# Performance work log

Measured on AMD Instinct MI355X. Metric: run time of the kernel, lower is better.

## Reference

```python
import jax, jax.numpy as jnp
import numpy as np

D_MODEL = 1024
N_HEADS = 16
D_HEAD = D_MODEL // N_HEADS
D_FF = 4096
BATCH = 2
SEQ = 2048
LN_EPS = 1e-5


def setup_inputs() -> dict:
    key = jax.random.key(0)
    ks = jax.random.split(key, 12)
    s = 1.0 / np.sqrt(D_MODEL)
    x = jax.random.normal(ks[0], (BATCH, SEQ, D_MODEL), dtype=jnp.float32)
    mask = jnp.broadcast_to(jnp.tril(jnp.ones((SEQ, SEQ), jnp.int32)), (BATCH, SEQ, SEQ))
    return {
        "x": x,
        "mask": mask,
        # per-head projections stacked: [H, D, Dh] (bias=False in source)
        "Wq": jax.random.normal(ks[1], (N_HEADS, D_MODEL, D_HEAD), jnp.float32) * s,
        "Wk": jax.random.normal(ks[2], (N_HEADS, D_MODEL, D_HEAD), jnp.float32) * s,
        "Wv": jax.random.normal(ks[3], (N_HEADS, D_MODEL, D_HEAD), jnp.float32) * s,
        "Wo": jax.random.normal(ks[4], (D_MODEL, D_MODEL), jnp.float32) * s,
        "ln1_w": jnp.ones((D_MODEL,), jnp.float32),
        "ln1_b": jnp.zeros((D_MODEL,), jnp.float32),
        "ln2_w": jnp.ones((D_MODEL,), jnp.float32),
        "ln2_b": jnp.zeros((D_MODEL,), jnp.float32),
        "W1": jax.random.normal(ks[5], (D_MODEL, D_FF), jnp.float32) * s,
        "b1": jnp.zeros((D_FF,), jnp.float32),
        "W2": jax.random.normal(ks[6], (D_FF, D_MODEL), jnp.float32) * (1.0 / np.sqrt(D_FF)),
        "b2": jnp.zeros((D_MODEL,), jnp.float32),
    }


def layer_norm(x, w, b):
    mu = jnp.mean(x, axis=-1, keepdims=True)
    var = jnp.var(x, axis=-1, keepdims=True)
    return (x - mu) * jax.lax.rsqrt(var + LN_EPS) * w + b


def reference(x, mask, Wq, Wk, Wv, Wo, ln1_w, ln1_b, ln2_w, ln2_b, W1, b1, W2, b2):
    # pre-LN masked self-attention
    h = layer_norm(x, ln1_w, ln1_b)
    q = jnp.einsum("bsd,hde->bhse", h, Wq)  # [B,H,S,Dh]
    k = jnp.einsum("bsd,hde->bhse", h, Wk)
    v = jnp.einsum("bsd,hde->bhse", h, Wv)
    scores = jnp.einsum("bhse,bhte->bhst", q, k) / np.sqrt(D_HEAD)
    scores = jnp.where(mask[:, None, :, :].astype(bool), scores, -jnp.inf)
    weights = jax.nn.softmax(scores, axis=-1)
    attn = jnp.einsum("bhst,bhte->bhse", weights, v)  # [B,H,S,Dh]
    # concat heads (head order = last-dim order in torch.cat)
    concat = attn.transpose(0, 2, 1, 3).reshape(x.shape[0], x.shape[1], D_MODEL)
    att_out = concat @ Wo
    att_x = x + att_out
    # FFN with exact (erf) GELU, matching nn.GELU default
    h2 = layer_norm(att_x, ln2_w, ln2_b)
    ff = jax.nn.gelu(h2 @ W1 + b1, approximate=False) @ W2 + b2
    return att_x + ff
```

## Files before the change

### kernel.cpp

```cpp
#include <hip/hip_runtime.h>
#include <hip/hip_bf16.h>
#include <math.h>

#define D_MODEL 1024
#define N_HEADS 16
#define D_HEAD  64
#define D_FF    4096
#define BATCH   2
#define SEQ     2048
#define NTOK    (BATCH*SEQ)

typedef __hip_bfloat16 bf16;
typedef __attribute__((ext_vector_type(8))) short short8;
typedef __attribute__((ext_vector_type(4))) float floatx4;

template<typename TIN>
__global__ void ln_kernel(const TIN* __restrict__ x,
                          const float* __restrict__ w,
                          const float* __restrict__ b,
                          bf16* __restrict__ out) {
    int row = blockIdx.x;
    int tid = threadIdx.x;
    const long base = (long)row * D_MODEL;
    float v[4];
    float s = 0.f, sq = 0.f;
#pragma unroll
    for (int i = 0; i < 4; ++i) {
        float xv = (float)x[base + tid + i*256];
        v[i] = xv; s += xv; sq += xv*xv;
    }
    __shared__ float r1[256], r2[256];
    r1[tid] = s; r2[tid] = sq; __syncthreads();
    for (int off = 128; off > 0; off >>= 1) {
        if (tid < off) { r1[tid] += r1[tid+off]; r2[tid] += r2[tid+off]; }
        __syncthreads();
    }
    float mean = r1[0] * (1.f/D_MODEL);
    float var  = r2[0] * (1.f/D_MODEL) - mean*mean;
    float rstd = rsqrtf(var + 1e-5f);
#pragma unroll
    for (int i = 0; i < 4; ++i) {
        int c = tid + i*256;
        out[base + c] = __float2bfloat16((v[i] - mean) * rstd * w[c] + b[c]);
    }
}

__global__ __launch_bounds__(256) void wcvt_kernel(const float* __restrict__ W,
                                                   bf16* __restrict__ Wt,
                                                   int K, int N) {
    __shared__ float t[32][33];
    int n0 = blockIdx.x * 32, k0 = blockIdx.y * 32;
    int lx = threadIdx.x & 31, ly = threadIdx.x >> 5;
#pragma unroll
    for (int i = 0; i < 4; ++i) {
        int k = ly + i * 8;
        t[k][lx] = W[(long)(k0 + k) * N + n0 + lx];
    }
    __syncthreads();
#pragma unroll
    for (int i = 0; i < 4; ++i) {
        int n = ly + i * 8;
        Wt[(long)(n0 + n) * K + k0 + lx] = __float2bfloat16(t[lx][n]);
    }
}

__global__ __launch_bounds__(256) void wcvt_wo_w1(const float* __restrict__ Wo,
                                                  const float* __restrict__ W1,
                                                  bf16* __restrict__ wo_bf,
                                                  bf16* __restrict__ w1_bf) {
    __shared__ float t[32][33];
    int gx = blockIdx.x;
    const float* W; bf16* Wt; int N, n0;
    if (gx < 32) { W = Wo; Wt = wo_bf; N = D_MODEL; n0 = gx * 32; }
    else         { W = W1; Wt = w1_bf; N = D_FF;    n0 = (gx - 32) * 32; }
    int k0 = blockIdx.y * 32;
    int lx = threadIdx.x & 31, ly = threadIdx.x >> 5;
#pragma unroll
    for (int i = 0; i < 4; ++i) {
        int k = ly + i * 8;
        t[k][lx] = W[(long)(k0 + k) * N + n0 + lx];
    }
    __syncthreads();
#pragma unroll
    for (int i = 0; i < 4; ++i) {
        int n = ly + i * 8;
        Wt[(long)(n0 + n) * D_MODEL + k0 + lx] = __float2bfloat16(t[lx][n]);
    }
}

__global__ __launch_bounds__(256) void wcvt_qkv(const float* __restrict__ Wq,
                                                const float* __restrict__ Wk,
                                                const float* __restrict__ Wv,
                                                bf16* __restrict__ outp) {
    __shared__ float t[32][33];
    int z = blockIdx.z, mat = z >> 4, head = z & 15;
    const float* W = (mat == 0 ? Wq : mat == 1 ? Wk : Wv) + (long)head * D_MODEL * D_HEAD;
    bf16* Wt = outp + (long)z * D_HEAD * D_MODEL;
    int n0 = blockIdx.x * 32, k0 = blockIdx.y * 32;
    int lx = threadIdx.x & 31, ly = threadIdx.x >> 5;
#pragma unroll
    for (int i = 0; i < 4; ++i) {
        int k = ly + i * 8;
        t[k][lx] = W[(long)(k0 + k) * D_HEAD + n0 + lx];
    }
    __syncthreads();
#pragma unroll
    for (int i = 0; i < 4; ++i) {
        int n = ly + i * 8;
        Wt[(long)(n0 + n) * D_MODEL + k0 + lx] = __float2bfloat16(t[lx][n]);
    }
}

__device__ inline void swz2d(int& bx, int& by) {
    int gx = gridDim.x;
    int nwg = gx * gridDim.y;
    int bid = blockIdx.y * gx + blockIdx.x;
    int swz = (bid & 7) * (nwg >> 3) + (bid >> 3);
    bx = swz % gx;
    by = swz / gx;
}

template<int ROWS>
__device__ inline void stage_tile(const bf16* g, int gstride, short* lds) {
    int lane = threadIdx.x & 63, wave = threadIdx.x >> 6;
#pragma unroll
    for (int it = 0; it < ROWS / 64; ++it) {
        int c = wave + it * 4;
        const bf16* gp = g + (long)(c * 16 + (lane >> 2)) * gstride + (lane & 3) * 8;
        short* lp = lds + c * 512 + lane * 8;
        __builtin_amdgcn_global_load_lds(
            (const __attribute__((address_space(1))) void*)gp,
            (__attribute__((address_space(3))) void*)lp, 16, 0, 0);
    }
}

template<int BM, int BN, int BK>
__device__ inline void gemm_accum(const bf16* __restrict__ A, int lda,
                                  const bf16* __restrict__ Wt, int K,
                                  int row0, int col0, short* As, short* Bs,
                                  floatx4 (&acc)[BM/32][BN/32]) {
    constexpr int MI  = BM / 32;
    constexpr int NR  = BN / 32;
    constexpr int ASZ = BM * BK;
    constexpr int BSZ = BN * BK;
    int tid  = threadIdx.x;
    int wave = tid >> 6, lane = tid & 63;
    int quad = lane >> 4, l16 = lane & 15;
    int wm = (wave >> 1) * (BM / 2);
    int wn = (wave & 1) * (BN / 2);

    auto stage = [&](int k0, int buf) {
#pragma unroll
        for (int kk = 0; kk < BK; kk += 32) {
            stage_tile<BM>(A  + (long)row0 * lda + k0 + kk, lda,
                           As + buf * ASZ + (kk / 32) * BM * 32);
            stage_tile<BN>(Wt + (long)col0 * K   + k0 + kk, K,
                           Bs + buf * BSZ + (kk / 32) * BN * 32);
        }
    };

    stage(0, 0);
    __syncthreads();

    int cur = 0;
    for (int k0 = 0; k0 < K; k0 += BK) {
        if (k0 + BK < K) stage(k0 + BK, cur ^ 1);

#pragma unroll
        for (int p = 0; p < BK / 32; ++p) {
            const short* Ap = As + cur * ASZ + p * BM * 32;
            const short* Bp = Bs + cur * BSZ + p * BN * 32;
            short8 af[MI], bfr[NR];
#pragma unroll
            for (int mi = 0; mi < MI; ++mi)
                af[mi] = *(const short8*)&Ap[(wm + mi * 16 + l16) * 32 + quad * 8];
#pragma unroll
            for (int ni = 0; ni < NR; ++ni)
                bfr[ni] = *(const short8*)&Bp[(wn + ni * 16 + l16) * 32 + quad * 8];
#pragma unroll
            for (int mi = 0; mi < MI; ++mi)
#pragma unroll
                for (int ni = 0; ni < NR; ++ni)
                    acc[mi][ni] = __builtin_amdgcn_mfma_f32_16x16x32_bf16(
                        af[mi], bfr[ni], acc[mi][ni], 0, 0, 0);
        }
        __syncthreads();
        cur ^= 1;
    }
}

template<int BM, int BN, int BK, int BIAS, int ACT, int RES, int OUTBF16>
__global__ __launch_bounds__(256) void mfma_gemm_bf(
    const bf16* __restrict__ A, int lda,
    const bf16* __restrict__ Wt, int K,
    const float* __restrict__ bias, const float* __restrict__ resid,
    void* __restrict__ Cout, int ldc)
{
    constexpr int MI = BM / 32;
    constexpr int NR = BN / 32;
    __shared__ short As[2 * BM * BK];
    __shared__ short Bs[2 * BN * BK];
    int bx, by; swz2d(bx, by);
    int row0 = by * BM, col0 = bx * BN;
    int tid = threadIdx.x, wave = tid >> 6, lane = tid & 63;
    int quad = lane >> 4, l16 = lane & 15;
    int wm = (wave >> 1) * (BM / 2);
    int wn = (wave & 1) * (BN / 2);

    floatx4 acc[MI][NR];
#pragma unroll
    for (int mi = 0; mi < MI; ++mi)
#pragma unroll
        for (int ni = 0; ni < NR; ++ni)
            acc[mi][ni] = (floatx4){0.f, 0.f, 0.f, 0.f};

    gemm_accum<BM, BN, BK>(A, lda, Wt, K, row0, col0, As, Bs, acc);

#pragma unroll
    for (int mi = 0; mi < MI; ++mi) {
#pragma unroll
        for (int ni = 0; ni < NR; ++ni) {
#pragma unroll
            for (int r = 0; r < 4; ++r) {
                int row = row0 + wm + mi * 16 + quad * 4 + r;
                int col = col0 + wn + ni * 16 + l16;
                float v = acc[mi][ni][r];
                if (BIAS) v += bias[col];
                if (ACT == 1) {
                    float x2 = v * v;
                    float arg = fminf(v * fmaf(0.1029392f, x2, 2.3021182f), 20.f);
                    float t = exp2f(arg);
                    v = v * t * __builtin_amdgcn_rcpf(t + 1.f);
                }
                long idx = (long)row * ldc + col;
                if (RES == 1) v += resid[idx];
                if (OUTBF16) ((bf16*)Cout)[idx] = __float2bfloat16(v);
                else         ((float*)Cout)[idx] = v;
            }
        }
    }
}

struct QkvOut { bf16* o[3]; };

#define RG(buf,mat,kh) (((buf)*4 + (mat)*2 + (kh)) * 8192)
#define G256_BAR  asm volatile("s_barrier" ::: "memory")
#define G256_VM4  asm volatile("s_waitcnt vmcnt(4)" ::: "memory")
#define G256_VM0  asm volatile("s_waitcnt vmcnt(0)" ::: "memory")
#define G256_LGKM0 do { asm volatile("s_waitcnt lgkmcnt(0)" ::: "memory"); \
                        __builtin_amdgcn_sched_barrier(0); } while (0)

__device__ inline void stage2(const bf16* g0, const bf16* g1, int koff, short* lp) {
    __builtin_amdgcn_global_load_lds(
        (const __attribute__((address_space(1))) void*)(g0 + koff),
        (__attribute__((address_space(3))) void*)lp, 16, 0, 0);
    __builtin_amdgcn_global_load_lds(
        (const __attribute__((address_space(1))) void*)(g1 + koff),
        (__attribute__((address_space(3))) void*)(lp + 4096), 16, 0, 0);
}

template<int MH>
__device__ inline void rd_frags_asm(unsigned ldsbase, int ra, int rb,
                                    const unsigned (&aoff)[8], const unsigned (&boff)[4],
                                    short8 (&areg)[4], short8 (&breg)[4]) {
    if (MH == 0) {
#pragma unroll
        for (int ni = 0; ni < 4; ++ni) {
            unsigned ad = ldsbase + (unsigned)(rb * 2) + boff[ni];
            asm volatile("ds_read_b128 %0, %1" : "=v"(breg[ni]) : "v"(ad));
        }
    }
#pragma unroll
    for (int mi = 0; mi < 4; ++mi) {
        unsigned ad = ldsbase + (unsigned)(ra * 2) + aoff[MH * 4 + mi];
        asm volatile("ds_read_b128 %0, %1" : "=v"(areg[mi]) : "v"(ad));
    }
}

template<int MH>
__device__ inline void do_mfma16(const short8 (&areg)[4], const short8 (&breg)[4],
                                 floatx4 (&acc)[8][4]) {
    __builtin_amdgcn_s_setprio(1);
#pragma unroll
    for (int mi = 0; mi < 4; ++mi)
#pragma unroll
        for (int ni = 0; ni < 4; ++ni)
            acc[MH * 4 + mi][ni] = __builtin_amdgcn_mfma_f32_16x16x32_bf16(
                areg[mi], breg[ni], acc[MH * 4 + mi][ni], 0, 0, 0);
    __builtin_amdgcn_s_setprio(0);
}

template<int EPI>
__global__ __launch_bounds__(512, 1) void gemm256_kernel(
    const bf16* __restrict__ A, int lda,
    const bf16* __restrict__ Wt, int ldw, int K,
    const float* __restrict__ bias,
    bf16* __restrict__ Cout, int ldc, QkvOut qa)
{
    __shared__ short lds[65536];
    const int NT = K / 64;
    int bx, by; swz2d(bx, by);
    int row0 = by * 256, col0 = bx * 256;
    int tid = threadIdx.x;
    int lane = tid & 63, wave = tid >> 6;
    int quad = lane >> 4, l16 = lane & 15;
    int wr = wave >> 2, wc = wave & 3;

    int srow = tid >> 2, slot = tid & 3;
    int cA0 = slot ^ ((srow >> 1) & 3);
    int cA1 = slot ^ (((srow + 128) >> 1) & 3);
    const bf16* a0 = A  + (long)(row0 + srow) * lda + cA0 * 8;
    const bf16* a1 = A  + (long)(row0 + srow + 128) * lda + cA1 * 8;
    const bf16* b0 = Wt + (long)(col0 + srow) * ldw + cA0 * 8;
    const bf16* b1 = Wt + (long)(col0 + srow + 128) * ldw + cA1 * 8;
    short* lt = lds + tid * 8;

    unsigned ldsbase = (unsigned)(unsigned long long)(void*)&lds[0];
    unsigned aoff[8], boff[4];
#pragma unroll
    for (int mi = 0; mi < 8; ++mi) {
        int row = wr * 128 + mi * 16 + l16;
        int sl = quad ^ ((row >> 1) & 3);
        aoff[mi] = (unsigned)((row * 32 + sl * 8) * 2);
    }
#pragma unroll
    for (int ni = 0; ni < 4; ++ni) {
        int row = wc * 64 + ni * 16 + l16;
        int sl = quad ^ ((row >> 1) & 3);
        boff[ni] = (unsigned)((row * 32 + sl * 8) * 2);
    }

    floatx4 acc[8][4];
#pragma unroll
    for (int mi = 0; mi < 8; ++mi)
#pragma unroll
        for (int ni = 0; ni < 4; ++ni)
            acc[mi][ni] = (floatx4){0.f, 0.f, 0.f, 0.f};

    stage2(a0, a1, 0,  lt + RG(0,0,0));
    stage2(b0, b1, 0,  lt + RG(0,1,0));
    stage2(a0, a1, 32, lt + RG(0,0,1));
    stage2(b0, b1, 32, lt + RG(0,1,1));
    stage2(a0, a1, 64, lt + RG(1,0,0));
    stage2(b0, b1, 64, lt + RG(1,1,0));
    G256_VM4;
    G256_BAR;

    short8 areg[4], breg[4];

    for (int i = 0; i < NT / 2; ++i) {
        int T = 2 * i;
        bool s2 = (T + 2 < NT);
        bool s3 = (T + 3 < NT);
        int k1off = (T + 1) * 64;
        int k2off = (T + 2) * 64;
        int k3off = (T + 3) * 64;

        rd_frags_asm<0>(ldsbase, RG(0,0,0), RG(0,1,0), aoff, boff, areg, breg);
        stage2(a0, a1, k1off + 32, lt + RG(1,0,1));
        G256_BAR;
        G256_LGKM0;
        do_mfma16<0>(areg, breg, acc);
        G256_BAR;

        rd_frags_asm<1>(ldsbase, RG(0,0,0), RG(0,1,0), aoff, boff, areg, breg);
        stage2(b0, b1, k1off + 32, lt + RG(1,1,1));
        G256_BAR;
        G256_LGKM0;
        do_mfma16<1>(areg, breg, acc);
        G256_BAR;

        rd_frags_asm<0>(ldsbase, RG(0,0,1), RG(0,1,1), aoff, boff, areg, breg);
        if (s2) stage2(a0, a1, k2off, lt + RG(0,0,0));
        G256_BAR;
        G256_LGKM0;
        do_mfma16<0>(areg, breg, acc);
        G256_BAR;

        rd_frags_asm<1>(ldsbase, RG(0,0,1), RG(0,1,1), aoff, boff, areg, breg);
        if (s2) stage2(b0, b1, k2off, lt + RG(0,1,0));
        G256_BAR;
        G256_LGKM0;
        do_mfma16<1>(areg, breg, acc);
        if (s2) { G256_VM4; } else { G256_VM0; }
        G256_BAR;

        rd_frags_asm<0>(ldsbase, RG(1,0,0), RG(1,1,0), aoff, boff, areg, breg);
        if (s2) stage2(a0, a1, k2off + 32, lt + RG(0,0,1));
        G256_BAR;
        G256_LGKM0;
        do_mfma16<0>(areg, breg, acc);
        G256_BAR;

        rd_frags_asm<1>(ldsbase, RG(1,0,0), RG(1,1,0), aoff, boff, areg, breg);
        if (s2) stage2(b0, b1, k2off + 32, lt + RG(0,1,1));
        G256_BAR;
        G256_LGKM0;
        do_mfma16<1>(areg, breg, acc);
        G256_BAR;

        rd_frags_asm<0>(ldsbase, RG(1,0,1), RG(1,1,1), aoff, boff, areg, breg);
        if (s3) stage2(a0, a1, k3off, lt + RG(1,0,0));
        G256_BAR;
        G256_LGKM0;
        do_mfma16<0>(areg, breg, acc);
        G256_BAR;

        rd_frags_asm<1>(ldsbase, RG(1,0,1), RG(1,1,1), aoff, boff, areg, breg);
        if (s3) stage2(b0, b1, k3off, lt + RG(1,1,0));
        G256_BAR;
        G256_LGKM0;
        do_mfma16<1>(areg, breg, acc);
        if (s3) { G256_VM4; } else { G256_VM0; }
        G256_BAR;
    }

#pragma unroll
    for (int mi = 0; mi < 8; ++mi) {
#pragma unroll
        for (int ni = 0; ni < 4; ++ni) {
#pragma unroll
            for (int r = 0; r < 4; ++r) {
                int row = row0 + wr * 128 + mi * 16 + quad * 4 + r;
                int col = col0 + wc * 64 + ni * 16 + l16;
                float v = acc[mi][ni][r];
                if constexpr (EPI == 0) {
                    v += bias[col];
                    float x2 = v * v;
                    float arg = fminf(v * fmaf(0.1029392f, x2, 2.3021182f), 20.f);
                    float t = exp2f(arg);
                    v = v * t * __builtin_amdgcn_rcpf(t + 1.f);
                    Cout[(long)row * ldc + col] = __float2bfloat16(v);
                } else {
                    int mat = col >> 10, hd = (col >> 6) & 15, d = col & 63;
                    int b = row >> 11, s = row & 2047;
                    qa.o[mat][(((long)(b * 16 + hd) * SEQ + s) << 6) + d] =
                        __float2bfloat16(v);
                }
            }
        }
    }
}

__global__ __launch_bounds__(256) void fattn_mfma(const bf16* __restrict__ q,
                                                  const bf16* __restrict__ k,
                                                  const bf16* __restrict__ v,
                                                  bf16* __restrict__ po,
                                                  float* __restrict__ lz) {
    int byr = blockIdx.y;
    int tile = (byr < 8) ? byr : 23 - byr;
    int chunk = blockIdx.z;
    int bh = blockIdx.x;
    int tid = threadIdx.x;
    int wave = tid >> 6, lane = tid & 63;
    int quad = lane >> 4, l16 = lane & 15;
    const long base = (long)bh * SEQ * D_HEAD;
    const int r0g = tile * 128;

    bf16*  pob = po + (long)chunk * 32 * SEQ * 64;
    float* lzb = lz + (long)chunk * 32 * SEQ;

    __shared__ short Ks[64 * 72];
    __shared__ short Vt[64 * 72];
    __shared__ short Ps[4][32 * 72];

    short8 qf[2][2];
#pragma unroll
    for (int rb = 0; rb < 2; ++rb) {
        const short* qrow = (const short*)(q + base +
            (long)(r0g + wave * 32 + rb * 16 + l16) * D_HEAD);
        qf[rb][0] = *(const short8*)(qrow + quad * 8);
        qf[rb][1] = *(const short8*)(qrow + 32 + quad * 8);
#pragma unroll
        for (int c = 0; c < 2; ++c)
#pragma unroll
            for (int j = 0; j < 8; ++j) {
                float f = __uint_as_float(((unsigned)(unsigned short)qf[rb][c][j]) << 16)
                          * 0.18033688f;
                qf[rb][c][j] = __builtin_bit_cast(short, __float2bfloat16(f));
            }
    }

    short8 onesf;
    {
        short o1 = (l16 == 0) ? (short)0x3F80 : (short)0;
#pragma unroll
        for (int j = 0; j < 8; ++j) onesf[j] = o1;
    }

    floatx4 o[2][4];
#pragma unroll
    for (int rb = 0; rb < 2; ++rb)
#pragma unroll
        for (int nb = 0; nb < 4; ++nb) o[rb][nb] = (floatx4){0.f, 0.f, 0.f, 0.f};
    floatx4 l4[2] = {(floatx4){0.f,0.f,0.f,0.f}, (floatx4){0.f,0.f,0.f,0.f}};

    const int kt0 = chunk ? tile + 1 : 0;
    const int kt1 = chunk ? 2 * tile + 1 : tile;
    for (int kt = kt0; kt <= kt1; ++kt) {
        __syncthreads();
        {
            int t = tid >> 2, c = tid & 3;
            const short* krow = (const short*)(k + base + (long)(kt * 64 + t) * D_HEAD);
            *(uint4*)&Ks[t * 72 + c * 16]     = *(const uint4*)(krow + c * 16);
            *(uint4*)&Ks[t * 72 + c * 16 + 8] = *(const uint4*)(krow + c * 16 + 8);
        }
        {
            int tp = (tid & 31) * 2;
            int d0 = ((tid >> 5) & 7) * 8;
            const short* v0 = (const short*)(v + base + (long)(kt * 64 + tp) * D_HEAD + d0);
            short va[8], vb[8];
            *(uint4*)va = *(const uint4*)v0;
            *(uint4*)vb = *(const uint4*)(v0 + D_HEAD);
#pragma unroll
            for (int j = 0; j < 8; ++j) {
                unsigned pk = (unsigned)(unsigned short)va[j] |
                              ((unsigned)(unsigned short)vb[j] << 16);
                *(unsigned*)&Vt[(d0 + j) * 72 + tp] = pk;
            }
        }
        __syncthreads();

        if (kt * 64 > r0g + wave * 32 + 31) continue;

        floatx4 s[2][4];
#pragma unroll
        for (int nb = 0; nb < 4; ++nb) {
            short8 kf0 = *(const short8*)&Ks[(nb * 16 + l16) * 72 + quad * 8];
            short8 kf1 = *(const short8*)&Ks[(nb * 16 + l16) * 72 + 32 + quad * 8];
#pragma unroll
            for (int rb = 0; rb < 2; ++rb) {
                floatx4 z4 = (floatx4){0.f, 0.f, 0.f, 0.f};
                z4 = __builtin_amdgcn_mfma_f32_16x16x32_bf16(qf[rb][0], kf0, z4, 0, 0, 0);
                z4 = __builtin_amdgcn_mfma_f32_16x16x32_bf16(qf[rb][1], kf1, z4, 0, 0, 0);
                s[rb][nb] = z4;
            }
        }

        if (kt >= 2 * tile) {
#pragma unroll
            for (int rb = 0; rb < 2; ++rb) {
                int qg = r0g + wave * 32 + rb * 16 + quad * 4;
#pragma unroll
                for (int nb = 0; nb < 4; ++nb) {
                    int kg = kt * 64 + nb * 16 + l16;
#pragma unroll
                    for (int r = 0; r < 4; ++r)
                        if (kg > qg + r) s[rb][nb][r] = -1e30f;
                }
            }
        }

        short* Pw = &Ps[wave][0];
#pragma unroll
        for (int rb = 0; rb < 2; ++rb)
#pragma unroll
            for (int nb = 0; nb < 4; ++nb)
#pragma unroll
                for (int r = 0; r < 4; ++r) {
                    float p = exp2f(s[rb][nb][r]);
                    Pw[(rb * 16 + quad * 4 + r) * 72 + nb * 16 + l16] =
                        __builtin_bit_cast(short, __float2bfloat16(p));
                }

        short8 pf[2][2];
#pragma unroll
        for (int rb = 0; rb < 2; ++rb) {
            pf[rb][0] = *(const short8*)&Pw[(rb * 16 + l16) * 72 + quad * 8];
            pf[rb][1] = *(const short8*)&Pw[(rb * 16 + l16) * 72 + 32 + quad * 8];
        }
#pragma unroll
        for (int nb = 0; nb < 4; ++nb) {
            short8 vf0 = *(const short8*)&Vt[(nb * 16 + l16) * 72 + quad * 8];
            short8 vf1 = *(const short8*)&Vt[(nb * 16 + l16) * 72 + 32 + quad * 8];
#pragma unroll
            for (int rb = 0; rb < 2; ++rb) {
                o[rb][nb] = __builtin_amdgcn_mfma_f32_16x16x32_bf16(pf[rb][0], vf0, o[rb][nb], 0, 0, 0);
                o[rb][nb] = __builtin_amdgcn_mfma_f32_16x16x32_bf16(pf[rb][1], vf1, o[rb][nb], 0, 0, 0);
            }
        }
#pragma unroll
        for (int rb = 0; rb < 2; ++rb) {
            l4[rb] = __builtin_amdgcn_mfma_f32_16x16x32_bf16(pf[rb][0], onesf, l4[rb], 0, 0, 0);
            l4[rb] = __builtin_amdgcn_mfma_f32_16x16x32_bf16(pf[rb][1], onesf, l4[rb], 0, 0, 0);
        }
    }

#pragma unroll
    for (int rb = 0; rb < 2; ++rb) {
#pragma unroll
        for (int nb = 0; nb < 4; ++nb)
#pragma unroll
            for (int r = 0; r < 4; ++r) {
                int row = r0g + wave * 32 + rb * 16 + quad * 4 + r;
                pob[((long)bh * SEQ + row) * 64 + nb * 16 + l16] =
                    __float2bfloat16(o[rb][nb][r]);
            }
        if (l16 == 0) {
#pragma unroll
            for (int r = 0; r < 4; ++r) {
                int row = r0g + wave * 32 + rb * 16 + quad * 4 + r;
                lzb[(long)bh * SEQ + row] = l4[rb][r];
            }
        }
    }
}

__global__ __launch_bounds__(256) void attn_combine(const bf16* __restrict__ po,
                                                    const float* __restrict__ lz,
                                                    bf16* __restrict__ cc) {
    const long CH = 32L * SEQ * 64;
    int row = blockIdx.x;
    int b = row >> 11, s = row & 2047;
    int tid = threadIdx.x;
    int col = tid * 4;
    int h = col >> 6, d = col & 63;
    long pidx = ((long)(b * 16 + h) * SEQ + s) * 64 + d;
    uint2 u0 = *(const uint2*)((const unsigned short*)po + pidx);
    uint2 u1 = *(const uint2*)((const unsigned short*)po + CH + pidx);
    long li = (long)(b * 16 + h) * SEQ + s;
    float linv = 1.f / (lz[li] + lz[32L * SEQ + li]);
    unsigned ua[4] = {u0.x & 0xFFFFu, u0.x >> 16, u0.y & 0xFFFFu, u0.y >> 16};
    unsigned ub[4] = {u1.x & 0xFFFFu, u1.x >> 16, u1.y & 0xFFFFu, u1.y >> 16};
    unsigned short rr[4];
#pragma unroll
    for (int i = 0; i < 4; ++i) {
        float ov = __uint_as_float(ua[i] << 16) + __uint_as_float(ub[i] << 16);
        rr[i] = __builtin_bit_cast(unsigned short, __float2bfloat16(ov * linv));
    }
    uint2 w;
    w.x = (unsigned)rr[0] | ((unsigned)rr[1] << 16);
    w.y = (unsigned)rr[2] | ((unsigned)rr[3] << 16);
    *(uint2*)((unsigned short*)cc + (long)row * D_MODEL + col) = w;
}

extern "C" void kernel_launch(void* const* d_in, const int* in_sizes, int n_in,
                              void* d_out, int out_size, void* d_ws, size_t ws_size,
                              hipStream_t stream) {
    const float* x    = (const float*)d_in[0];
    const float* Wq   = (const float*)d_in[2];
    const float* Wk   = (const float*)d_in[3];
    const float* Wv   = (const float*)d_in[4];
    const float* Wo   = (const float*)d_in[5];
    const float* ln1w = (const float*)d_in[6];
    const float* ln1b = (const float*)d_in[7];
    const float* ln2w = (const float*)d_in[8];
    const float* ln2b = (const float*)d_in[9];
    const float* W1   = (const float*)d_in[10];
    const float* b1   = (const float*)d_in[11];
    const float* W2   = (const float*)d_in[12];
    const float* b2   = (const float*)d_in[13];
    float* out = (float*)d_out;

    char* wsb = (char*)d_ws;
    const size_t MB = 1024*1024;
    bf16*  h1      = (bf16*)(wsb + 0*MB);
    bf16*  qb      = (bf16*)(wsb + 8*MB);
    bf16*  kb      = (bf16*)(wsb + 16*MB);
    bf16*  vb      = (bf16*)(wsb + 24*MB);
    bf16*  wqkv_bf = (bf16*)(wsb + 32*MB);
    bf16*  po      = (bf16*)(wsb + 32*MB);
    float* lz      = (float*)(wsb + 48*MB);
    bf16*  cc      = (bf16*)(wsb + 0*MB);
    bf16*  wo_bf   = (bf16*)(wsb + 8*MB);
    bf16*  w1_bf   = (bf16*)(wsb + 10*MB);
    bf16*  h2      = (bf16*)(wsb + 0*MB);
    bf16*  ff      = (bf16*)(wsb + 24*MB);
    bf16*  w2_bf   = (bf16*)(wsb + 8*MB);

    QkvOut qa; qa.o[0] = qb; qa.o[1] = kb; qa.o[2] = vb;
    QkvOut qdummy = {};

    ln_kernel<float><<<NTOK, 256, 0, stream>>>(x, ln1w, ln1b, h1);

    wcvt_qkv<<<dim3(2, 32, 48), 256, 0, stream>>>(Wq, Wk, Wv, wqkv_bf);

    gemm256_kernel<1><<<dim3(12, 16), 512, 0, stream>>>(
        h1, D_MODEL, wqkv_bf, D_MODEL, D_MODEL, nullptr, nullptr, 0, qa);

    fattn_mfma<<<dim3(BATCH*N_HEADS, SEQ/128, 2), 256, 0, stream>>>(qb, kb, vb, po, lz);

    attn_combine<<<NTOK, 256, 0, stream>>>(po, lz, cc);

    wcvt_wo_w1<<<dim3(160, 32), 256, 0, stream>>>(Wo, W1, wo_bf, w1_bf);

    mfma_gemm_bf<64,128,64,0,0,1,0><<<dim3(8,64), 256, 0, stream>>>(
        cc, D_MODEL, wo_bf, D_MODEL, nullptr, x, out, D_MODEL);

    ln_kernel<float><<<NTOK, 256, 0, stream>>>(out, ln2w, ln2b, h2);

    gemm256_kernel<0><<<dim3(16, 16), 512, 0, stream>>>(
        h2, D_MODEL, w1_bf, D_MODEL, D_MODEL, b1, ff, D_FF, qdummy);

    wcvt_kernel<<<dim3(D_MODEL/32, D_FF/32), 256, 0, stream>>>(W2, w2_bf, D_FF, D_MODEL);

    mfma_gemm_bf<64,128,64,1,0,1,0><<<dim3(8,64), 256, 0, stream>>>(
        ff, D_FF, w2_bf, D_FF, b2, out, out, D_MODEL);
}
```

Baseline: 373.5 us.

## Add triple-buffered LDS pipeline GEMM for FFN down-projection

Adds a new GEMM kernel that keeps three K-tiles in flight in LDS using direct global-to-LDS loads, with explicit vmcnt waits and raw ds_read_b128 fragment reads. It is used only for the W2 down-projection (K=4096), replacing the double-buffered kernel. The aim is to hide global memory latency on this long-K GEMM. In exchange it uses more LDS per block, which may reduce occupancy.

```diff
diff --git a/kernel.cpp b/kernel.cpp
--- a/kernel.cpp
+++ b/kernel.cpp
@@ -132,6 +132,20 @@
             (const __attribute__((address_space(1))) void*)gp,
             (__attribute__((address_space(3))) void*)lp, 16, 0, 0);
     }
+}
+
+#define G256_BAR  asm volatile("s_barrier" ::: "memory")
+#define G256_VM12 asm volatile("s_waitcnt vmcnt(12)" ::: "memory")
+#define G256_VM6  asm volatile("s_waitcnt vmcnt(6)" ::: "memory")
+#define G256_VM4  asm volatile("s_waitcnt vmcnt(4)" ::: "memory")
+#define G256_VM0  asm volatile("s_waitcnt vmcnt(0)" ::: "memory")
+#define G256_LGKM0 do { asm volatile("s_waitcnt lgkmcnt(0)" ::: "memory"); \
+                        __builtin_amdgcn_sched_barrier(0); } while (0)
+
+__device__ inline short8 rd128(unsigned ad) {
+    short8 r;
+    asm volatile("ds_read_b128 %0, %1" : "=v"(r) : "v"(ad));
+    return r;
 }
 
 template<int BM, int BN, int BK>
@@ -241,14 +255,119 @@
     }
 }
 
+template<int BM, int BN, int BK, int BIAS, int ACT, int RES, int OUTBF16>
+__global__ __launch_bounds__(256) void mfma_gemm_pipe3(
+    const bf16* __restrict__ A, int lda,
+    const bf16* __restrict__ Wt, int K,
+    const float* __restrict__ bias, const float* __restrict__ resid,
+    void* __restrict__ Cout, int ldc)
+{
+    constexpr int MI  = BM / 32;
+    constexpr int NR  = BN / 32;
+    constexpr int ASZ = BM * BK;
+    constexpr int BSZ = BN * BK;
+    __shared__ short As[3 * BM * BK];
+    __shared__ short Bs[3 * BN * BK];
+    int bx, by; swz2d(bx, by);
+    int row0 = by * BM, col0 = bx * BN;
+    int tid = threadIdx.x, wave = tid >> 6, lane = tid & 63;
+    int quad = lane >> 4, l16 = lane & 15;
+    int wm = (wave >> 1) * (BM / 2);
+    int wn = (wave & 1) * (BN / 2);
+    const int NT = K / BK;
+
+    auto stage = [&](int t, int buf) {
+        int k0 = t * BK;
+#pragma unroll
+        for (int kk = 0; kk < BK; kk += 32) {
+            stage_tile<BM>(A  + (long)row0 * lda + k0 + kk, lda,
+                           As + buf * ASZ + (kk / 32) * BM * 32);
+            stage_tile<BN>(Wt + (long)col0 * K   + k0 + kk, K,
+                           Bs + buf * BSZ + (kk / 32) * BN * 32);
+        }
+    };
+
+    unsigned asbase = (unsigned)(unsigned long long)(void*)&As[0];
+    unsigned bsbase = (unsigned)(unsigned long long)(void*)&Bs[0];
+    unsigned aRow[MI], bRow[NR];
+#pragma unroll
+    for (int mi = 0; mi < MI; ++mi)
+        aRow[mi] = (unsigned)(((wm + mi * 16 + l16) * 32 + quad * 8) * 2);
+#pragma unroll
+    for (int ni = 0; ni < NR; ++ni)
+        bRow[ni] = (unsigned)(((wn + ni * 16 + l16) * 32 + quad * 8) * 2);
+
+    floatx4 acc[MI][NR];
+#pragma unroll
+    for (int mi = 0; mi < MI; ++mi)
+#pragma unroll
+        for (int ni = 0; ni < NR; ++ni)
+            acc[mi][ni] = (floatx4){0.f, 0.f, 0.f, 0.f};
+
+    stage(0, 0);
+    if (NT > 1) stage(1, 1);
+    if (NT > 2) stage(2, 2);
+
+    int buf = 0;
+    for (int i = 0; i < NT; ++i) {
+        if (i + 2 < NT)      { G256_VM12; }
+        else if (i + 1 < NT) { G256_VM6;  }
+        else                 { G256_VM0;  }
+        G256_BAR;
+
+        short8 af[BK / 32][MI], bfr[BK / 32][NR];
+#pragma unroll
+        for (int p = 0; p < BK / 32; ++p) {
+            unsigned ab = asbase + (unsigned)((buf * ASZ + p * BM * 32) * 2);
+            unsigned bb = bsbase + (unsigned)((buf * BSZ + p * BN * 32) * 2);
+#pragma unroll
+            for (int mi = 0; mi < MI; ++mi) af[p][mi] = rd128(ab + aRow[mi]);
+#pragma unroll
+            for (int ni = 0; ni < NR; ++ni) bfr[p][ni] = rd128(bb + bRow[ni]);
+        }
+        G256_LGKM0;
+#pragma unroll
+        for (int p = 0; p < BK / 32; ++p)
+#pragma unroll
+            for (int mi = 0; mi < MI; ++mi)
+#pragma unroll
+                for (int ni = 0; ni < NR; ++ni)
+                    acc[mi][ni] = __builtin_amdgcn_mfma_f32_16x16x32_bf16(
+                        af[p][mi], bfr[p][ni], acc[mi][ni], 0, 0, 0);
+
+        G256_BAR;
+        if (i + 3 < NT) stage(i + 3, buf);
+        buf = (buf == 2) ? 0 : buf + 1;
+    }
+
+#pragma unroll
+    for (int mi = 0; mi < MI; ++mi) {
+#pragma unroll
+        for (int ni = 0; ni < NR; ++ni) {
+#pragma unroll
+            for (int r = 0; r < 4; ++r) {
+                int row = row0 + wm + mi * 16 + quad * 4 + r;
+                int col = col0 + wn + ni * 16 + l16;
+                float v = acc[mi][ni][r];
+                if (BIAS) v += bias[col];
+                if (ACT == 1) {
+                    float x2 = v * v;
+                    float arg = fminf(v * fmaf(0.1029392f, x2, 2.3021182f), 20.f);
+                    float t = exp2f(arg);
+                    v = v * t * __builtin_amdgcn_rcpf(t + 1.f);
+                }
+                long idx = (long)row * ldc + col;
+                if (RES == 1) v += resid[idx];
+                if (OUTBF16) ((bf16*)Cout)[idx] = __float2bfloat16(v);
+                else         ((float*)Cout)[idx] = v;
+            }
+        }
+    }
+}
+
 struct QkvOut { bf16* o[3]; };
 
 #define RG(buf,mat,kh) (((buf)*4 + (mat)*2 + (kh)) * 8192)
-#define G256_BAR  asm volatile("s_barrier" ::: "memory")
-#define G256_VM4  asm volatile("s_waitcnt vmcnt(4)" ::: "memory")
-#define G256_VM0  asm volatile("s_waitcnt vmcnt(0)" ::: "memory")
-#define G256_LGKM0 do { asm volatile("s_waitcnt lgkmcnt(0)" ::: "memory"); \
-                        __builtin_amdgcn_sched_barrier(0); } while (0)
 
 __device__ inline void stage2(const bf16* g0, const bf16* g1, int koff, short* lp) {
     __builtin_amdgcn_global_load_lds(
@@ -694,6 +813,6 @@
 
     wcvt_kernel<<<dim3(D_MODEL/32, D_FF/32), 256, 0, stream>>>(W2, w2_bf, D_FF, D_MODEL);
 
-    mfma_gemm_bf<64,128,64,1,0,1,0><<<dim3(8,64), 256, 0, stream>>>(
+    mfma_gemm_pipe3<64,128,64,1,0,1,0><<<dim3(8,64), 256, 0, stream>>>(
         ff, D_FF, w2_bf, D_FF, b2, out, out, D_MODEL);
 }
```

Result: faster. 360.3 us (-3.5%).

## Triple-buffer Wo/W2 GEMMs and prefetch K/V tiles in flash attention

Applied to the files above, without the earlier changes.

Replaces the double-buffered 64x128 GEMM used for the Wo and W2 projections with a three-stage pipeline. It uses explicit vmcnt waits, raw ds_read_b128 fragment loads and restaging after the compute barrier, so two tiles are in flight while one is computed. In the attention kernel, the next K/V tile is loaded into registers during the current iteration, and s_setprio is raised around the MFMA blocks. This trades more LDS and register use, which may lower occupancy, for hiding global-load latency.

```diff
diff --git a/kernel.cpp b/kernel.cpp
--- a/kernel.cpp
+++ b/kernel.cpp
@@ -134,78 +134,61 @@
     }
 }
 
-template<int BM, int BN, int BK>
-__device__ inline void gemm_accum(const bf16* __restrict__ A, int lda,
-                                  const bf16* __restrict__ Wt, int K,
-                                  int row0, int col0, short* As, short* Bs,
-                                  floatx4 (&acc)[BM/32][BN/32]) {
-    constexpr int MI  = BM / 32;
-    constexpr int NR  = BN / 32;
-    constexpr int ASZ = BM * BK;
-    constexpr int BSZ = BN * BK;
-    int tid  = threadIdx.x;
-    int wave = tid >> 6, lane = tid & 63;
-    int quad = lane >> 4, l16 = lane & 15;
-    int wm = (wave >> 1) * (BM / 2);
-    int wn = (wave & 1) * (BN / 2);
-
-    auto stage = [&](int k0, int buf) {
-#pragma unroll
-        for (int kk = 0; kk < BK; kk += 32) {
-            stage_tile<BM>(A  + (long)row0 * lda + k0 + kk, lda,
-                           As + buf * ASZ + (kk / 32) * BM * 32);
-            stage_tile<BN>(Wt + (long)col0 * K   + k0 + kk, K,
-                           Bs + buf * BSZ + (kk / 32) * BN * 32);
-        }
-    };
-
-    stage(0, 0);
-    __syncthreads();
-
-    int cur = 0;
-    for (int k0 = 0; k0 < K; k0 += BK) {
-        if (k0 + BK < K) stage(k0 + BK, cur ^ 1);
-
-#pragma unroll
-        for (int p = 0; p < BK / 32; ++p) {
-            const short* Ap = As + cur * ASZ + p * BM * 32;
-            const short* Bp = Bs + cur * BSZ + p * BN * 32;
-            short8 af[MI], bfr[NR];
-#pragma unroll
-            for (int mi = 0; mi < MI; ++mi)
-                af[mi] = *(const short8*)&Ap[(wm + mi * 16 + l16) * 32 + quad * 8];
-#pragma unroll
-            for (int ni = 0; ni < NR; ++ni)
-                bfr[ni] = *(const short8*)&Bp[(wn + ni * 16 + l16) * 32 + quad * 8];
-#pragma unroll
-            for (int mi = 0; mi < MI; ++mi)
-#pragma unroll
-                for (int ni = 0; ni < NR; ++ni)
-                    acc[mi][ni] = __builtin_amdgcn_mfma_f32_16x16x32_bf16(
-                        af[mi], bfr[ni], acc[mi][ni], 0, 0, 0);
-        }
-        __syncthreads();
-        cur ^= 1;
-    }
+#define G256_BAR  asm volatile("s_barrier" ::: "memory")
+#define G256_VM12 asm volatile("s_waitcnt vmcnt(12)" ::: "memory")
+#define G256_VM6  asm volatile("s_waitcnt vmcnt(6)" ::: "memory")
+#define G256_VM4  asm volatile("s_waitcnt vmcnt(4)" ::: "memory")
+#define G256_VM0  asm volatile("s_waitcnt vmcnt(0)" ::: "memory")
+#define G256_LGKM0 do { asm volatile("s_waitcnt lgkmcnt(0)" ::: "memory"); \
+                        __builtin_amdgcn_sched_barrier(0); } while (0)
+
+__device__ inline short8 rd128(unsigned ad) {
+    short8 r;
+    asm volatile("ds_read_b128 %0, %1" : "=v"(r) : "v"(ad));
+    return r;
 }
 
 template<int BM, int BN, int BK, int BIAS, int ACT, int RES, int OUTBF16>
-__global__ __launch_bounds__(256) void mfma_gemm_bf(
+__global__ __launch_bounds__(256) void mfma_gemm_pipe3(
     const bf16* __restrict__ A, int lda,
     const bf16* __restrict__ Wt, int K,
     const float* __restrict__ bias, const float* __restrict__ resid,
     void* __restrict__ Cout, int ldc)
 {
-    constexpr int MI = BM / 32;
-    constexpr int NR = BN / 32;
-    __shared__ short As[2 * BM * BK];
-    __shared__ short Bs[2 * BN * BK];
+    constexpr int MI  = BM / 32;
+    constexpr int NR  = BN / 32;
+    constexpr int ASZ = BM * BK;
+    constexpr int BSZ = BN * BK;
+    __shared__ short As[3 * BM * BK];
+    __shared__ short Bs[3 * BN * BK];
     int bx, by; swz2d(bx, by);
     int row0 = by * BM, col0 = bx * BN;
     int tid = threadIdx.x, wave = tid >> 6, lane = tid & 63;
     int quad = lane >> 4, l16 = lane & 15;
     int wm = (wave >> 1) * (BM / 2);
     int wn = (wave & 1) * (BN / 2);
+    const int NT = K / BK;
+
+    auto stage = [&](int t, int buf) {
+        int k0 = t * BK;
+#pragma unroll
+        for (int kk = 0; kk < BK; kk += 32) {
+            stage_tile<BM>(A  + (long)row0 * lda + k0 + kk, lda,
+                           As + buf * ASZ + (kk / 32) * BM * 32);
+            stage_tile<BN>(Wt + (long)col0 * K   + k0 + kk, K,
+                           Bs + buf * BSZ + (kk / 32) * BN * 32);
+        }
+    };
+
+    unsigned asbase = (unsigned)(unsigned long long)(void*)&As[0];
+    unsigned bsbase = (unsigned)(unsigned long long)(void*)&Bs[0];
+    unsigned aRow[MI], bRow[NR];
+#pragma unroll
+    for (int mi = 0; mi < MI; ++mi)
+        aRow[mi] = (unsigned)(((wm + mi * 16 + l16) * 32 + quad * 8) * 2);
+#pragma unroll
+    for (int ni = 0; ni < NR; ++ni)
+        bRow[ni] = (unsigned)(((wn + ni * 16 + l16) * 32 + quad * 8) * 2);
 
     floatx4 acc[MI][NR];
 #pragma unroll
@@ -214,7 +197,41 @@
         for (int ni = 0; ni < NR; ++ni)
             acc[mi][ni] = (floatx4){0.f, 0.f, 0.f, 0.f};
 
-    gemm_accum<BM, BN, BK>(A, lda, Wt, K, row0, col0, As, Bs, acc);
+    stage(0, 0);
+    if (NT > 1) stage(1, 1);
+    if (NT > 2) stage(2, 2);
+
+    int buf = 0;
+    for (int i = 0; i < NT; ++i) {
+        if (i + 2 < NT)      { G256_VM12; }
+        else if (i + 1 < NT) { G256_VM6;  }
+        else                 { G256_VM0;  }
+        G256_BAR;
+
+        short8 af[BK / 32][MI], bfr[BK / 32][NR];
+#pragma unroll
+        for (int p = 0; p < BK / 32; ++p) {
+            unsigned ab = asbase + (unsigned)((buf * ASZ + p * BM * 32) * 2);
+            unsigned bb = bsbase + (unsigned)((buf * BSZ + p * BN * 32) * 2);
+#pragma unroll
+            for (int mi = 0; mi < MI; ++mi) af[p][mi] = rd128(ab + aRow[mi]);
+#pragma unroll
+            for (int ni = 0; ni < NR; ++ni) bfr[p][ni] = rd128(bb + bRow[ni]);
+        }
+        G256_LGKM0;
+#pragma unroll
+        for (int p = 0; p < BK / 32; ++p)
+#pragma unroll
+            for (int mi = 0; mi < MI; ++mi)
+#pragma unroll
+                for (int ni = 0; ni < NR; ++ni)
+                    acc[mi][ni] = __builtin_amdgcn_mfma_f32_16x16x32_bf16(
+                        af[p][mi], bfr[p][ni], acc[mi][ni], 0, 0, 0);
+
+        G256_BAR;
+        if (i + 3 < NT) stage(i + 3, buf);
+        buf = (buf == 2) ? 0 : buf + 1;
+    }
 
 #pragma unroll
     for (int mi = 0; mi < MI; ++mi) {
@@ -244,11 +261,6 @@
 struct QkvOut { bf16* o[3]; };
 
 #define RG(buf,mat,kh) (((buf)*4 + (mat)*2 + (kh)) * 8192)
-#define G256_BAR  asm volatile("s_barrier" ::: "memory")
-#define G256_VM4  asm volatile("s_waitcnt vmcnt(4)" ::: "memory")
-#define G256_VM0  asm volatile("s_waitcnt vmcnt(0)" ::: "memory")
-#define G256_LGKM0 do { asm volatile("s_waitcnt lgkmcnt(0)" ::: "memory"); \
-                        __builtin_amdgcn_sched_barrier(0); } while (0)
 
 __device__ inline void stage2(const bf16* g0, const bf16* g1, int koff, short* lp) {
     __builtin_amdgcn_global_load_lds(
@@ -497,21 +509,36 @@
 
     const int kt0 = chunk ? tile + 1 : 0;
     const int kt1 = chunk ? 2 * tile + 1 : tile;
+
+    uint4 kr0, kr1, va4, vb4;
+    auto ldKV = [&](int kt) {
+        const short* krow = (const short*)(k + base +
+            (long)(kt * 64 + (tid >> 2)) * D_HEAD);
+        int c = tid & 3;
+        kr0 = *(const uint4*)(krow + c * 16);
+        kr1 = *(const uint4*)(krow + c * 16 + 8);
+        int tp = (tid & 31) * 2;
+        int d0 = ((tid >> 5) & 7) * 8;
+        const short* v0 = (const short*)(v + base + (long)(kt * 64 + tp) * D_HEAD + d0);
+        va4 = *(const uint4*)v0;
+        vb4 = *(const uint4*)(v0 + D_HEAD);
+    };
+
+    ldKV(kt0);
+
     for (int kt = kt0; kt <= kt1; ++kt) {
         __syncthreads();
         {
             int t = tid >> 2, c = tid & 3;
-            const short* krow = (const short*)(k + base + (long)(kt * 64 + t) * D_HEAD);
-            *(uint4*)&Ks[t * 72 + c * 16]     = *(const uint4*)(krow + c * 16);
-            *(uint4*)&Ks[t * 72 + c * 16 + 8] = *(const uint4*)(krow + c * 16 + 8);
+            *(uint4*)&Ks[t * 72 + c * 16]     = kr0;
+            *(uint4*)&Ks[t * 72 + c * 16 + 8] = kr1;
         }
         {
             int tp = (tid & 31) * 2;
             int d0 = ((tid >> 5) & 7) * 8;
-            const short* v0 = (const short*)(v + base + (long)(kt * 64 + tp) * D_HEAD + d0);
             short va[8], vb[8];
-            *(uint4*)va = *(const uint4*)v0;
-            *(uint4*)vb = *(const uint4*)(v0 + D_HEAD);
+            *(uint4*)va = va4;
+            *(uint4*)vb = vb4;
 #pragma unroll
             for (int j = 0; j < 8; ++j) {
                 unsigned pk = (unsigned)(unsigned short)va[j] |
@@ -519,11 +546,13 @@
                 *(unsigned*)&Vt[(d0 + j) * 72 + tp] = pk;
             }
         }
+        if (kt < kt1) ldKV(kt + 1);
         __syncthreads();
 
         if (kt * 64 > r0g + wave * 32 + 31) continue;
 
         floatx4 s[2][4];
+        __builtin_amdgcn_s_setprio(1);
 #pragma unroll
         for (int nb = 0; nb < 4; ++nb) {
             short8 kf0 = *(const short8*)&Ks[(nb * 16 + l16) * 72 + quad * 8];
@@ -536,6 +565,7 @@
                 s[rb][nb] = z4;
             }
         }
+        __builtin_amdgcn_s_setprio(0);
 
         if (kt >= 2 * tile) {
 #pragma unroll
@@ -569,6 +599,7 @@
             pf[rb][0] = *(const short8*)&Pw[(rb * 16 + l16) * 72 + quad * 8];
             pf[rb][1] = *(const short8*)&Pw[(rb * 16 + l16) * 72 + 32 + quad * 8];
         }
+        __builtin_amdgcn_s_setprio(1);
 #pragma unroll
         for (int nb = 0; nb < 4; ++nb) {
             short8 vf0 = *(const short8*)&Vt[(nb * 16 + l16) * 72 + quad * 8];
@@ -584,6 +615,7 @@
             l4[rb] = __builtin_amdgcn_mfma_f32_16x16x32_bf16(pf[rb][0], onesf, l4[rb], 0, 0, 0);
             l4[rb] = __builtin_amdgcn_mfma_f32_16x16x32_bf16(pf[rb][1], onesf, l4[rb], 0, 0, 0);
         }
+        __builtin_amdgcn_s_setprio(0);
     }
 
 #pragma unroll
@@ -684,7 +716,7 @@
 
     wcvt_wo_w1<<<dim3(160, 32), 256, 0, stream>>>(Wo, W1, wo_bf, w1_bf);
 
-    mfma_gemm_bf<64,128,64,0,0,1,0><<<dim3(8,64), 256, 0, stream>>>(
+    mfma_gemm_pipe3<64,128,64,0,0,1,0><<<dim3(8,64), 256, 0, stream>>>(
         cc, D_MODEL, wo_bf, D_MODEL, nullptr, x, out, D_MODEL);
 
     ln_kernel<float><<<NTOK, 256, 0, stream>>>(out, ln2w, ln2b, h2);
@@ -694,6 +726,6 @@
 
     wcvt_kernel<<<dim3(D_MODEL/32, D_FF/32), 256, 0, stream>>>(W2, w2_bf, D_FF, D_MODEL);
 
-    mfma_gemm_bf<64,128,64,1,0,1,0><<<dim3(8,64), 256, 0, stream>>>(
+    mfma_gemm_pipe3<64,128,64,1,0,1,0><<<dim3(8,64), 256, 0, stream>>>(
         ff, D_FF, w2_bf, D_FF, b2, out, out, D_MODEL);
 }
```

Result: faster. 358.8 us (-3.9%).
